# Kernel tuning notes

Hardware: AMD Instinct MI355X
Metric: run time of the kernel (lower is better)

The kernel has to match this reference:

```python
import jax, jax.numpy as jnp
import numpy as np

VOCAB = 100000
EMB = 300
HID = 512            # bidirectional total; per-direction = 256
HD = HID // 2
TAGS = 12
START = 10
STOP = 11
NEG = -10000.0
T = 4096


def _lstm_dir(x, h0, c0, Wih, Whh, bih, bhh, reverse):
    # x: [T, EMB]; PyTorch gate order i, f, g, o
    def step(carry, xt):
        h, c = carry
        g = xt @ Wih.T + h @ Whh.T + bih + bhh           # [4*HD]
        i, f, gg, o = jnp.split(g, 4)
        i = jax.nn.sigmoid(i); f = jax.nn.sigmoid(f)
        gg = jnp.tanh(gg); o = jax.nn.sigmoid(o)
        c = f * c + i * gg
        h = o * jnp.tanh(c)
        return (h, c), h
    _, hs = jax.lax.scan(step, (h0, c0), x, reverse=reverse)
    return hs                                            # [T, HD]


def setup_inputs() -> dict:
    key = jax.random.key(0)
    ks = jax.random.split(key, 16)
    s = 0.05  # weight scale for numerical stability
    sentence = jax.random.randint(ks[0], (T,), 0, VOCAB)
    h0 = jax.random.normal(ks[1], (2, HD), jnp.float32)
    c0 = jax.random.normal(ks[2], (2, HD), jnp.float32)
    embed = jax.random.normal(ks[3], (VOCAB, EMB), jnp.float32) * s
    W_ih_f = jax.random.normal(ks[4], (4 * HD, EMB), jnp.float32) * s
    W_hh_f = jax.random.normal(ks[5], (4 * HD, HD), jnp.float32) * s
    b_ih_f = jax.random.normal(ks[6], (4 * HD,), jnp.float32) * s
    b_hh_f = jax.random.normal(ks[7], (4 * HD,), jnp.float32) * s
    W_ih_b = jax.random.normal(ks[8], (4 * HD, EMB), jnp.float32) * s
    W_hh_b = jax.random.normal(ks[9], (4 * HD, HD), jnp.float32) * s
    b_ih_b = jax.random.normal(ks[10], (4 * HD,), jnp.float32) * s
    b_hh_b = jax.random.normal(ks[11], (4 * HD,), jnp.float32) * s
    W_tag = jax.random.normal(ks[12], (TAGS, HID), jnp.float32) * s
    b_tag = jax.random.normal(ks[13], (TAGS,), jnp.float32) * s
    transitions = jax.random.normal(ks[14], (TAGS, TAGS), jnp.float32)
    transitions = transitions.at[START, :].set(NEG).at[:, STOP].set(NEG)
    return dict(sentence=sentence, h0=h0, c0=c0, embed=embed,
                W_ih_f=W_ih_f, W_hh_f=W_hh_f, b_ih_f=b_ih_f, b_hh_f=b_hh_f,
                W_ih_b=W_ih_b, W_hh_b=W_hh_b, b_ih_b=b_ih_b, b_hh_b=b_hh_b,
                W_tag=W_tag, b_tag=b_tag, transitions=transitions)


def reference(sentence, h0, c0, embed,
              W_ih_f, W_hh_f, b_ih_f, b_hh_f,
              W_ih_b, W_hh_b, b_ih_b, b_hh_b,
              W_tag, b_tag, transitions):
    # --- BiLSTM features (dropout layers are identity at inference) ---
    x = embed[sentence]                                      # [T, EMB]
    hf = _lstm_dir(x, h0[0], c0[0], W_ih_f, W_hh_f, b_ih_f, b_hh_f, False)
    hb = _lstm_dir(x, h0[1], c0[1], W_ih_b, W_hh_b, b_ih_b, b_hh_b, True)
    feats = jnp.concatenate([hf, hb], axis=-1) @ W_tag.T + b_tag  # [T, TAGS]

    # --- Viterbi decode: transitions[to, from] ---
    init = jnp.full((TAGS,), NEG, jnp.float32).at[START].set(0.0)

    def vstep(fv, feat):
        ntv = fv[None, :] + transitions                      # [to, from]
        bp = jnp.argmax(ntv, axis=1)                         # best prev tag per 'to'
        fv2 = jnp.max(ntv, axis=1) + feat
        return fv2, bp

    fv, bps = jax.lax.scan(vstep, init, feats)               # bps: [T, TAGS]
    terminal = fv + transitions[STOP]
    best = jnp.argmax(terminal)
    path_score = terminal[best]

    def back(tag, bp):
        return bp[tag], tag

    _, best_path = jax.lax.scan(back, best, bps, reverse=True)  # [T] tags in time order
    return path_score, best_path
```

## Files before the change

### kernel.cpp

```cpp
#include <hip/hip_runtime.h>

#define T_LEN 4096
#define EMB   300
#define HD    256
#define G4    1024
#define N2    2048
#define TAGS  12
#define NEGV  -10000.0f
#define SENT  0x7F7F7F7Fu

__global__ __launch_bounds__(256) void gin_gemm(
    const int* __restrict__ sent, const float* __restrict__ embed,
    const float* __restrict__ Wf, const float* __restrict__ Wb,
    const float* __restrict__ bihf, const float* __restrict__ bhhf,
    const float* __restrict__ bihb, const float* __restrict__ bhhb,
    float* __restrict__ gin)
{
    __shared__ float AsT[32][68];
    __shared__ float BsT[32][68];
    __shared__ int   sIdx[64];
    const int tid = threadIdx.x;
    const int bn = blockIdx.x;
    const int bm = blockIdx.y;
    if (tid < 64) sIdx[tid] = sent[bm*64 + tid];
    __syncthreads();

    float acc[4][4] = {};
    const int lr = tid >> 3;
    const int lk = (tid & 7) << 2;
    const int m0 = (tid >> 4) << 2;
    const int n0 = (tid & 15) << 2;

    for (int kc = 0; kc < 10; ++kc) {
        const int k0 = kc*32 + lk;
        #pragma unroll
        for (int h = 0; h < 2; ++h) {
            const int row = lr + h*32;
            float4 va = make_float4(0.f,0.f,0.f,0.f);
            if (k0 + 3 < EMB)
                va = *(const float4*)(embed + (long)sIdx[row]*EMB + k0);
            AsT[lk+0][row]=va.x; AsT[lk+1][row]=va.y;
            AsT[lk+2][row]=va.z; AsT[lk+3][row]=va.w;

            const int rn = bn*64 + row;
            const float* bsrc = (rn < G4) ? (Wf + (long)rn*EMB) : (Wb + (long)(rn-G4)*EMB);
            float4 vb = make_float4(0.f,0.f,0.f,0.f);
            if (k0 + 3 < EMB)
                vb = *(const float4*)(bsrc + k0);
            BsT[lk+0][row]=vb.x; BsT[lk+1][row]=vb.y;
            BsT[lk+2][row]=vb.z; BsT[lk+3][row]=vb.w;
        }
        __syncthreads();
        #pragma unroll
        for (int kk = 0; kk < 32; ++kk) {
            const float4 a4 = *(const float4*)&AsT[kk][m0];
            const float4 b4 = *(const float4*)&BsT[kk][n0];
            const float a[4] = {a4.x, a4.y, a4.z, a4.w};
            const float b[4] = {b4.x, b4.y, b4.z, b4.w};
            #pragma unroll
            for (int i = 0; i < 4; ++i)
                #pragma unroll
                for (int jj = 0; jj < 4; ++jj)
                    acc[i][jj] = fmaf(a[i], b[jj], acc[i][jj]);
        }
        __syncthreads();
    }

    #pragma unroll
    for (int i = 0; i < 4; ++i) {
        const int t = bm*64 + m0 + i;
        #pragma unroll
        for (int jj = 0; jj < 4; ++jj) {
            const int r = bn*64 + n0 + jj;
            const float bias = (r < G4) ? (bihf[r] + bhhf[r])
                                        : (bihb[r-G4] + bhhb[r-G4]);
            gin[(long)t*N2 + r] = acc[i][jj] + bias;
        }
    }
}

#define MV(K) { const float4 hv = h4[K];                    \
    a0 = fmaf(wA##K.x, hv.x, a0);                           \
    a1 = fmaf(wA##K.y, hv.y, a1);                           \
    a2 = fmaf(wA##K.z, hv.z, a2);                           \
    a3 = fmaf(wA##K.w, hv.w, a3); }

__global__ __launch_bounds__(1024) __attribute__((amdgpu_waves_per_eu(4, 4)))
void lstm_persist(
    const float* Whh_f, const float* Whh_b,
    const float* __restrict__ h0, const float* __restrict__ c0,
    const float* __restrict__ gin,
    float* Hh)
{
    const int blk = blockIdx.x;
    const int m8  = blk & 7;
    if (m8 != 0 && m8 != 4) return;
    const int dir = (m8 == 4);
    const int b   = blk >> 3;
    const int tid = threadIdx.x;
    const int u     = tid & 63;
    const int wvid  = tid >> 6;
    const int gate  = wvid >> 2;
    const int q     = wvid & 3;
    const int unit0 = b*64;
    const int row   = gate*64 + u;
    const int grow  = gate*HD + unit0 + u;

    const float4* W4 = (const float4*)((dir ? Whh_b : Whh_f)
                                       + (long)grow*HD + q*64);
    const float4 wA0  = W4[0],  wA1  = W4[1],  wA2  = W4[2],  wA3  = W4[3];
    const float4 wA4  = W4[4],  wA5  = W4[5],  wA6  = W4[6],  wA7  = W4[7];
    const float4 wA8  = W4[8],  wA9  = W4[9],  wA10 = W4[10], wA11 = W4[11];
    const float4 wA12 = W4[12], wA13 = W4[13], wA14 = W4[14], wA15 = W4[15];

    __shared__ __align__(16) float hS[20480];
    __shared__ float ps[3][256];
    __shared__ float gvS[256];

    float cst = 0.f;
    if (tid < 64) cst = c0[dir*HD + unit0 + tid];
    if (tid < HD) hS[tid] = h0[dir*HD + tid];

    const float* ginD = gin + dir*G4;
    float gx = (q == 0) ? ginD[(long)(dir ? T_LEN-1 : 0)*N2 + grow] : 0.f;

    #pragma unroll 1
    for (int s = 0; s < T_LEN; ++s) {
        const int t = dir ? (T_LEN-1-s) : s;
        float gxn = 0.f;
        if (q == 0 && s+1 < T_LEN)
            gxn = ginD[(long)(dir ? t-1 : t+1)*N2 + grow];

        __syncthreads();
        const float4* h4 = (const float4*)(hS + q*64);
        float a0=0.f, a1=0.f, a2=0.f, a3=0.f;
        MV(0)  MV(1)  MV(2)  MV(3)
        MV(4)  MV(5)  MV(6)  MV(7)
        MV(8)  MV(9)  MV(10) MV(11)
        MV(12) MV(13) MV(14) MV(15)
        const float a = (a0+a1)+(a2+a3);

        if (q != 0) ps[q-1][row] = a;
        __syncthreads();

        if (q == 0) {
            const float raw = a + ps[0][row] + ps[1][row] + ps[2][row] + gx;
            gvS[row] = (gate == 2) ? tanhf(raw) : 1.f/(1.f + expf(-raw));
        }
        __syncthreads();

        if (tid < 64) {
            const float i_ = gvS[tid],       f_ = gvS[64+tid];
            const float g_ = gvS[128+tid],   o_ = gvS[192+tid];
            cst = fmaf(f_, cst, i_*g_);
            const float hv = o_ * tanhf(cst);
            hS[unit0 + tid] = hv;
            __hip_atomic_store(&Hh[(long)t*512 + dir*HD + unit0 + tid], hv,
                               __ATOMIC_RELAXED, __HIP_MEMORY_SCOPE_AGENT);
        } else if (tid < 256 && s+1 < T_LEN) {
            const int fidx = tid - 64;
            const int gu   = (fidx < unit0) ? fidx : fidx + 64;
            const long idx = (long)t*512 + dir*HD + gu;
            float v;
            do {
                v = __hip_atomic_load(&Hh[idx], __ATOMIC_RELAXED,
                                      __HIP_MEMORY_SCOPE_AGENT);
            } while (__float_as_uint(v) == SENT);
            hS[gu] = v;
        }
        gx = gxn;
    }
}

__global__ __launch_bounds__(192) void feats_kernel(
    const float* __restrict__ Hhist, const float* __restrict__ Wtag,
    const float* __restrict__ btag, float* __restrict__ feats)
{
    __shared__ __align__(16) float Ws[TAGS][512];
    const int tid = threadIdx.x;
    for (int i = tid; i < TAGS*512; i += 192) Ws[0][i] = Wtag[i];
    __syncthreads();
    const int tl = tid / TAGS;
    const int tg = tid % TAGS;
    const int t  = blockIdx.x * 16 + tl;
    const float4* hrow = (const float4*)(Hhist + (long)t*512);
    const float4* wrow = (const float4*)(&Ws[tg][0]);
    float a0=0.f,a1=0.f,a2=0.f,a3=0.f;
    #pragma unroll 8
    for (int k = 0; k < 128; ++k) {
        const float4 h = hrow[k];
        const float4 ww = wrow[k];
        a0=fmaf(h.x,ww.x,a0); a1=fmaf(h.y,ww.y,a1);
        a2=fmaf(h.z,ww.z,a2); a3=fmaf(h.w,ww.w,a3);
    }
    feats[t*TAGS + tg] = ((a0+a1)+(a2+a3)) + btag[tg];
}

__global__ __launch_bounds__(256) void viterbi_kernel(
    const float* __restrict__ feats, const float* __restrict__ trans,
    float* __restrict__ out)
{
    __shared__ float fS[256*TAGS];
    __shared__ unsigned char bps[T_LEN*TAGS];
    __shared__ float fvS[TAGS];
    const int tid = threadIdx.x;

    float tr[TAGS];
    float fv = NEGV;
    if (tid < TAGS) {
        #pragma unroll
        for (int f = 0; f < TAGS; ++f) tr[f] = trans[tid*TAGS + f];
        fv = (tid == 10) ? 0.f : NEGV;
    }

    for (int c = 0; c < T_LEN/256; ++c) {
        __syncthreads();
        for (int i = tid; i < 256*TAGS; i += 256) fS[i] = feats[c*256*TAGS + i];
        __syncthreads();
        if (tid < TAGS) {
            for (int s = 0; s < 256; ++s) {
                float best = -3.4e38f; int bp = 0;
                #pragma unroll
                for (int f = 0; f < TAGS; ++f) {
                    const float v = __shfl(fv, f, 64) + tr[f];
                    if (v > best) { best = v; bp = f; }
                }
                bps[(c*256+s)*TAGS + tid] = (unsigned char)bp;
                fv = best + fS[s*TAGS + tid];
            }
        }
    }
    __syncthreads();
    if (tid < TAGS) fvS[tid] = fv + trans[11*TAGS + tid];
    __syncthreads();
    if (tid == 0) {
        float bestv = fvS[0]; int best = 0;
        #pragma unroll
        for (int g = 1; g < TAGS; ++g) if (fvS[g] > bestv) { bestv = fvS[g]; best = g; }
        out[0] = bestv;
        int cur = best;
        for (int t = T_LEN-1; t >= 0; --t) {
            out[1+t] = (float)cur;
            cur = bps[t*TAGS + cur];
        }
    }
}

extern "C" void kernel_launch(void* const* d_in, const int* in_sizes, int n_in,
                              void* d_out, int out_size, void* d_ws, size_t ws_size,
                              hipStream_t stream)
{
    (void)in_sizes; (void)n_in; (void)out_size; (void)ws_size;
    const int*   sentence = (const int*)  d_in[0];
    const float* h0       = (const float*)d_in[1];
    const float* c0       = (const float*)d_in[2];
    const float* embed    = (const float*)d_in[3];
    const float* Wihf     = (const float*)d_in[4];
    const float* Whhf     = (const float*)d_in[5];
    const float* bihf     = (const float*)d_in[6];
    const float* bhhf     = (const float*)d_in[7];
    const float* Wihb     = (const float*)d_in[8];
    const float* Whhb     = (const float*)d_in[9];
    const float* bihb     = (const float*)d_in[10];
    const float* bhhb     = (const float*)d_in[11];
    const float* Wtag     = (const float*)d_in[12];
    const float* btag     = (const float*)d_in[13];
    const float* trans    = (const float*)d_in[14];
    float* out = (float*)d_out;

    float* gin   = (float*)d_ws;
    float* Hh    = gin + (long)T_LEN*N2;
    float* feats = Hh  + (long)T_LEN*512;

    hipMemsetAsync(Hh, 0x7F, (size_t)T_LEN*512*sizeof(float), stream);

    dim3 ggrid(32, 64);
    gin_gemm<<<ggrid, 256, 0, stream>>>(sentence, embed, Wihf, Wihb,
                                        bihf, bhhf, bihb, bhhb, gin);
    lstm_persist<<<29, 1024, 0, stream>>>(Whhf, Whhb, h0, c0, gin, Hh);
    feats_kernel<<<T_LEN/16, 192, 0, stream>>>(Hh, Wtag, btag, feats);
    viterbi_kernel<<<1, 256, 0, stream>>>(feats, trans, out);
}
```

Before: 7.204 ms.

## Split LSTM recurrence by K-slices across blocks and exchange partial sums

The recurrent matvec is repartitioned so each of four blocks per direction owns a 64-wide slice of the hidden input for all 1024 gate rows, instead of owning 64 output units. Blocks exchange partial dot products through a ring of global slots guarded by sentinels. Each block then redundantly computes the full gate nonlinearity and cell update locally, which drops the per-step all-gather of hidden state and one intra-block barrier. In exchange every block polls three remote partial buffers each step. Slot reuse correctness rests on a sentinel written eight steps ahead.

```diff
diff --git a/kernel.cpp b/kernel.cpp
--- a/kernel.cpp
+++ b/kernel.cpp
@@ -8,6 +8,7 @@
 #define TAGS  12
 #define NEGV  -10000.0f
 #define SENT  0x7F7F7F7Fu
+#define NSLOT 16
 
 __global__ __launch_bounds__(256) void gin_gemm(
     const int* __restrict__ sent, const float* __restrict__ embed,
@@ -85,12 +86,13 @@
     a2 = fmaf(wA##K.z, hv.z, a2);                           \
     a3 = fmaf(wA##K.w, hv.w, a3); }
 
-__global__ __launch_bounds__(1024) __attribute__((amdgpu_waves_per_eu(4, 4)))
+__global__ __launch_bounds__(1024, 4)
 void lstm_persist(
-    const float* Whh_f, const float* Whh_b,
+    const float* __restrict__ Whh_f, const float* __restrict__ Whh_b,
     const float* __restrict__ h0, const float* __restrict__ c0,
     const float* __restrict__ gin,
-    float* Hh)
+    float* __restrict__ Hh,
+    float* __restrict__ Pbuf)
 {
     const int blk = blockIdx.x;
     const int m8  = blk & 7;
@@ -98,41 +100,40 @@
     const int dir = (m8 == 4);
     const int b   = blk >> 3;
     const int tid = threadIdx.x;
-    const int u     = tid & 63;
-    const int wvid  = tid >> 6;
-    const int gate  = wvid >> 2;
-    const int q     = wvid & 3;
-    const int unit0 = b*64;
-    const int row   = gate*64 + u;
-    const int grow  = gate*HD + unit0 + u;
+    const int gate = tid >> 8;
 
     const float4* W4 = (const float4*)((dir ? Whh_b : Whh_f)
-                                       + (long)grow*HD + q*64);
+                                       + (long)tid*HD + b*64);
     const float4 wA0  = W4[0],  wA1  = W4[1],  wA2  = W4[2],  wA3  = W4[3];
     const float4 wA4  = W4[4],  wA5  = W4[5],  wA6  = W4[6],  wA7  = W4[7];
     const float4 wA8  = W4[8],  wA9  = W4[9],  wA10 = W4[10], wA11 = W4[11];
     const float4 wA12 = W4[12], wA13 = W4[13], wA14 = W4[14], wA15 = W4[15];
 
     __shared__ __align__(16) float hS[20480];
-    __shared__ float ps[3][256];
-    __shared__ float gvS[256];
+    __shared__ float gvS[G4];
 
     float cst = 0.f;
-    if (tid < 64) cst = c0[dir*HD + unit0 + tid];
-    if (tid < HD) hS[tid] = h0[dir*HD + tid];
+    if (tid < HD) {
+        cst = c0[dir*HD + tid];
+        hS[tid] = h0[dir*HD + tid];
+    }
+    __syncthreads();
 
     const float* ginD = gin + dir*G4;
-    float gx = (q == 0) ? ginD[(long)(dir ? T_LEN-1 : 0)*N2 + grow] : 0.f;
+    float gx = ginD[(long)(dir ? T_LEN-1 : 0)*N2 + tid];
+
+    const int f0 = (b == 0) ? 1 : 0;
+    const int f1 = (b <= 1) ? 2 : 1;
+    const int f2 = (b <= 2) ? 3 : 2;
 
     #pragma unroll 1
     for (int s = 0; s < T_LEN; ++s) {
         const int t = dir ? (T_LEN-1-s) : s;
         float gxn = 0.f;
-        if (q == 0 && s+1 < T_LEN)
-            gxn = ginD[(long)(dir ? t-1 : t+1)*N2 + grow];
-
-        __syncthreads();
-        const float4* h4 = (const float4*)(hS + q*64);
+        if (s+1 < T_LEN)
+            gxn = ginD[(long)(dir ? t-1 : t+1)*N2 + tid];
+
+        const float4* h4 = (const float4*)(hS + b*64);
         float a0=0.f, a1=0.f, a2=0.f, a3=0.f;
         MV(0)  MV(1)  MV(2)  MV(3)
         MV(4)  MV(5)  MV(6)  MV(7)
@@ -140,34 +141,48 @@
         MV(12) MV(13) MV(14) MV(15)
         const float a = (a0+a1)+(a2+a3);
 
-        if (q != 0) ps[q-1][row] = a;
-        __syncthreads();
-
-        if (q == 0) {
-            const float raw = a + ps[0][row] + ps[1][row] + ps[2][row] + gx;
-            gvS[row] = (gate == 2) ? tanhf(raw) : 1.f/(1.f + expf(-raw));
-        }
-        __syncthreads();
-
-        if (tid < 64) {
-            const float i_ = gvS[tid],       f_ = gvS[64+tid];
-            const float g_ = gvS[128+tid],   o_ = gvS[192+tid];
+        const long sb  = ((long)((s & (NSLOT-1))*2 + dir))*4096;
+        const long sbf = ((long)((((s+8) & (NSLOT-1))*2) + dir))*4096;
+        __hip_atomic_store(&Pbuf[sb  + b*1024 + tid], a,
+                           __ATOMIC_RELAXED, __HIP_MEMORY_SCOPE_AGENT);
+        __hip_atomic_store(&Pbuf[sbf + b*1024 + tid], __uint_as_float(SENT),
+                           __ATOMIC_RELAXED, __HIP_MEMORY_SCOPE_AGENT);
+
+        float* P0 = Pbuf + sb + f0*1024 + tid;
+        float* P1 = Pbuf + sb + f1*1024 + tid;
+        float* P2 = Pbuf + sb + f2*1024 + tid;
+        float v0 = 0.f, v1 = 0.f, v2 = 0.f;
+        bool d0 = false, d1 = false, d2 = false;
+        do {
+            if (!d0) { v0 = __hip_atomic_load(P0, __ATOMIC_RELAXED,
+                                              __HIP_MEMORY_SCOPE_AGENT);
+                       d0 = (__float_as_uint(v0) != SENT); }
+            if (!d1) { v1 = __hip_atomic_load(P1, __ATOMIC_RELAXED,
+                                              __HIP_MEMORY_SCOPE_AGENT);
+                       d1 = (__float_as_uint(v1) != SENT); }
+            if (!d2) { v2 = __hip_atomic_load(P2, __ATOMIC_RELAXED,
+                                              __HIP_MEMORY_SCOPE_AGENT);
+                       d2 = (__float_as_uint(v2) != SENT); }
+        } while (!(d0 && d1 && d2));
+
+        const float pos0 = (b == 0) ? a : v0;
+        const float pos1 = (b == 1) ? a : ((b == 0) ? v0 : v1);
+        const float pos2 = (b == 2) ? a : ((b <= 1) ? v1 : v2);
+        const float pos3 = (b == 3) ? a : v2;
+        const float g = ((pos0 + pos1) + (pos2 + pos3)) + gx;
+        gvS[tid] = (gate == 2) ? tanhf(g) : 1.f/(1.f + expf(-g));
+        __syncthreads();
+
+        if (tid < HD) {
+            const float i_ = gvS[tid],        f_ = gvS[HD + tid];
+            const float g_ = gvS[2*HD + tid], o_ = gvS[3*HD + tid];
             cst = fmaf(f_, cst, i_*g_);
             const float hv = o_ * tanhf(cst);
-            hS[unit0 + tid] = hv;
-            __hip_atomic_store(&Hh[(long)t*512 + dir*HD + unit0 + tid], hv,
-                               __ATOMIC_RELAXED, __HIP_MEMORY_SCOPE_AGENT);
-        } else if (tid < 256 && s+1 < T_LEN) {
-            const int fidx = tid - 64;
-            const int gu   = (fidx < unit0) ? fidx : fidx + 64;
-            const long idx = (long)t*512 + dir*HD + gu;
-            float v;
-            do {
-                v = __hip_atomic_load(&Hh[idx], __ATOMIC_RELAXED,
-                                      __HIP_MEMORY_SCOPE_AGENT);
-            } while (__float_as_uint(v) == SENT);
-            hS[gu] = v;
-        }
+            hS[tid] = hv;
+            if (b == 0)
+                Hh[(long)t*512 + dir*HD + tid] = hv;
+        }
+        __syncthreads();
         gx = gxn;
     }
 }
@@ -269,15 +284,16 @@
     float* out = (float*)d_out;
 
     float* gin   = (float*)d_ws;
-    float* Hh    = gin + (long)T_LEN*N2;
-    float* feats = Hh  + (long)T_LEN*512;
-
-    hipMemsetAsync(Hh, 0x7F, (size_t)T_LEN*512*sizeof(float), stream);
+    float* Hh    = gin   + (long)T_LEN*N2;
+    float* feats = Hh    + (long)T_LEN*512;
+    float* Pbuf  = feats + (long)T_LEN*TAGS;
+
+    hipMemsetAsync(Pbuf, 0x7F, (size_t)NSLOT*2*4*1024*sizeof(float), stream);
 
     dim3 ggrid(32, 64);
     gin_gemm<<<ggrid, 256, 0, stream>>>(sentence, embed, Wihf, Wihb,
                                         bihf, bhhf, bihb, bhhb, gin);
-    lstm_persist<<<29, 1024, 0, stream>>>(Whhf, Whhb, h0, c0, gin, Hh);
+    lstm_persist<<<29, 1024, 0, stream>>>(Whhf, Whhb, h0, c0, gin, Hh, Pbuf);
     feats_kernel<<<T_LEN/16, 192, 0, stream>>>(Hh, Wtag, btag, feats);
     viterbi_kernel<<<1, 256, 0, stream>>>(feats, trans, out);
 }
```

New measurement: 9.777 ms. 1.36x slower.

## Fuse input-projection GEMM into persistent LSTM kernel with sentinel-polled readiness

Applied to the files above, without the earlier changes.

Merges the input-gate GEMM and the persistent recurrent LSTM into one launch. Extra blocks compute GEMM tiles in an order alternating from both ends of the sequence, so the forward and backward directions get their early timesteps first. The recurrent blocks poll gin for a sentinel value before using it, which lets the GEMM overlap the serial recurrence and removes the separate GEMM launch. The trade-offs are a full gin memset, atomic loads and spin loops in the recurrence, and 145KB of shared memory for every block. GEMM blocks now use 1024 threads each computing a 2x2 tile, and there is a forward-progress risk if the LSTM blocks are not scheduled before the GEMM blocks.

```diff
diff --git a/kernel.cpp b/kernel.cpp
--- a/kernel.cpp
+++ b/kernel.cpp
@@ -8,76 +8,7 @@
 #define TAGS  12
 #define NEGV  -10000.0f
 #define SENT  0x7F7F7F7Fu
-
-__global__ __launch_bounds__(256) void gin_gemm(
-    const int* __restrict__ sent, const float* __restrict__ embed,
-    const float* __restrict__ Wf, const float* __restrict__ Wb,
-    const float* __restrict__ bihf, const float* __restrict__ bhhf,
-    const float* __restrict__ bihb, const float* __restrict__ bhhb,
-    float* __restrict__ gin)
-{
-    __shared__ float AsT[32][68];
-    __shared__ float BsT[32][68];
-    __shared__ int   sIdx[64];
-    const int tid = threadIdx.x;
-    const int bn = blockIdx.x;
-    const int bm = blockIdx.y;
-    if (tid < 64) sIdx[tid] = sent[bm*64 + tid];
-    __syncthreads();
-
-    float acc[4][4] = {};
-    const int lr = tid >> 3;
-    const int lk = (tid & 7) << 2;
-    const int m0 = (tid >> 4) << 2;
-    const int n0 = (tid & 15) << 2;
-
-    for (int kc = 0; kc < 10; ++kc) {
-        const int k0 = kc*32 + lk;
-        #pragma unroll
-        for (int h = 0; h < 2; ++h) {
-            const int row = lr + h*32;
-            float4 va = make_float4(0.f,0.f,0.f,0.f);
-            if (k0 + 3 < EMB)
-                va = *(const float4*)(embed + (long)sIdx[row]*EMB + k0);
-            AsT[lk+0][row]=va.x; AsT[lk+1][row]=va.y;
-            AsT[lk+2][row]=va.z; AsT[lk+3][row]=va.w;
-
-            const int rn = bn*64 + row;
-            const float* bsrc = (rn < G4) ? (Wf + (long)rn*EMB) : (Wb + (long)(rn-G4)*EMB);
-            float4 vb = make_float4(0.f,0.f,0.f,0.f);
-            if (k0 + 3 < EMB)
-                vb = *(const float4*)(bsrc + k0);
-            BsT[lk+0][row]=vb.x; BsT[lk+1][row]=vb.y;
-            BsT[lk+2][row]=vb.z; BsT[lk+3][row]=vb.w;
-        }
-        __syncthreads();
-        #pragma unroll
-        for (int kk = 0; kk < 32; ++kk) {
-            const float4 a4 = *(const float4*)&AsT[kk][m0];
-            const float4 b4 = *(const float4*)&BsT[kk][n0];
-            const float a[4] = {a4.x, a4.y, a4.z, a4.w};
-            const float b[4] = {b4.x, b4.y, b4.z, b4.w};
-            #pragma unroll
-            for (int i = 0; i < 4; ++i)
-                #pragma unroll
-                for (int jj = 0; jj < 4; ++jj)
-                    acc[i][jj] = fmaf(a[i], b[jj], acc[i][jj]);
-        }
-        __syncthreads();
-    }
-
-    #pragma unroll
-    for (int i = 0; i < 4; ++i) {
-        const int t = bm*64 + m0 + i;
-        #pragma unroll
-        for (int jj = 0; jj < 4; ++jj) {
-            const int r = bn*64 + n0 + jj;
-            const float bias = (r < G4) ? (bihf[r] + bhhf[r])
-                                        : (bihb[r-G4] + bhhb[r-G4]);
-            gin[(long)t*N2 + r] = acc[i][jj] + bias;
-        }
-    }
-}
+#define NLSTM 29
 
 #define MV(K) { const float4 hv = h4[K];                    \
     a0 = fmaf(wA##K.x, hv.x, a0);                           \
@@ -85,19 +16,87 @@
     a2 = fmaf(wA##K.z, hv.z, a2);                           \
     a3 = fmaf(wA##K.w, hv.w, a3); }
 
-__global__ __launch_bounds__(1024) __attribute__((amdgpu_waves_per_eu(4, 4)))
-void lstm_persist(
+__global__ __launch_bounds__(1024) void fused_gemm_lstm(
+    const int* __restrict__ sent, const float* __restrict__ embed,
+    const float* __restrict__ Wihf, const float* __restrict__ Wihb,
+    const float* __restrict__ bihf, const float* __restrict__ bhhf,
+    const float* __restrict__ bihb, const float* __restrict__ bhhb,
     const float* Whh_f, const float* Whh_b,
     const float* __restrict__ h0, const float* __restrict__ c0,
-    const float* __restrict__ gin,
+    float* gin,
     float* Hh)
 {
+    __shared__ __align__(16) char smem[145*1024];
     const int blk = blockIdx.x;
-    const int m8  = blk & 7;
+    const int tid = threadIdx.x;
+
+    if (blk >= NLSTM) {
+        float* AsT  = (float*)smem;
+        float* BsT  = (float*)(smem + 8704);
+        int*   sIdx = (int*)  (smem + 17408);
+        const int g  = blk - NLSTM;
+        const int kk8 = g >> 5;
+        const int bn  = g & 31;
+        const int bm  = (kk8 & 1) ? (63 - (kk8 >> 1)) : (kk8 >> 1);
+
+        if (tid < 64) sIdx[tid] = sent[bm*64 + tid];
+        __syncthreads();
+
+        const int srow = tid >> 4;
+        const int skj  = (tid & 15) << 1;
+        const int m0   = (tid >> 5) << 1;
+        const int n0   = (tid & 31) << 1;
+        const int rn   = bn * 64;
+        float acc00=0.f, acc01=0.f, acc10=0.f, acc11=0.f;
+
+        for (int kc = 0; kc < 10; ++kc) {
+            const int k0 = kc*32 + skj;
+            float2 va = make_float2(0.f, 0.f), vb = make_float2(0.f, 0.f);
+            if (k0 + 1 < EMB) {
+                va = *(const float2*)(embed + (long)sIdx[srow]*EMB + k0);
+                const int r = rn + srow;
+                const float* bsrc = (r < G4) ? (Wihf + (long)r*EMB)
+                                             : (Wihb + (long)(r-G4)*EMB);
+                vb = *(const float2*)(bsrc + k0);
+            }
+            AsT[skj*68 + srow]     = va.x;
+            AsT[(skj+1)*68 + srow] = va.y;
+            BsT[skj*68 + srow]     = vb.x;
+            BsT[(skj+1)*68 + srow] = vb.y;
+            __syncthreads();
+            #pragma unroll
+            for (int kk = 0; kk < 32; ++kk) {
+                const float2 a2v = *(const float2*)&AsT[kk*68 + m0];
+                const float2 b2v = *(const float2*)&BsT[kk*68 + n0];
+                acc00 = fmaf(a2v.x, b2v.x, acc00);
+                acc01 = fmaf(a2v.x, b2v.y, acc01);
+                acc10 = fmaf(a2v.y, b2v.x, acc10);
+                acc11 = fmaf(a2v.y, b2v.y, acc11);
+            }
+            __syncthreads();
+        }
+
+        const int c0i = rn + n0, c1i = c0i + 1;
+        const float bias0 = (c0i < G4) ? (bihf[c0i] + bhhf[c0i])
+                                       : (bihb[c0i-G4] + bhhb[c0i-G4]);
+        const float bias1 = (c1i < G4) ? (bihf[c1i] + bhhf[c1i])
+                                       : (bihb[c1i-G4] + bhhb[c1i-G4]);
+        const long t0 = (long)(bm*64 + m0), t1 = t0 + 1;
+        __hip_atomic_store(&gin[t0*N2 + c0i], acc00 + bias0,
+                           __ATOMIC_RELAXED, __HIP_MEMORY_SCOPE_AGENT);
+        __hip_atomic_store(&gin[t0*N2 + c1i], acc01 + bias1,
+                           __ATOMIC_RELAXED, __HIP_MEMORY_SCOPE_AGENT);
+        __hip_atomic_store(&gin[t1*N2 + c0i], acc10 + bias0,
+                           __ATOMIC_RELAXED, __HIP_MEMORY_SCOPE_AGENT);
+        __hip_atomic_store(&gin[t1*N2 + c1i], acc11 + bias1,
+                           __ATOMIC_RELAXED, __HIP_MEMORY_SCOPE_AGENT);
+        return;
+    }
+
+    const int m8 = blk & 7;
     if (m8 != 0 && m8 != 4) return;
     const int dir = (m8 == 4);
     const int b   = blk >> 3;
-    const int tid = threadIdx.x;
     const int u     = tid & 63;
     const int wvid  = tid >> 6;
     const int gate  = wvid >> 2;
@@ -106,6 +105,10 @@
     const int row   = gate*64 + u;
     const int grow  = gate*HD + unit0 + u;
 
+    float* hS  = (float*)smem;
+    float* ps  = (float*)(smem + 1024);
+    float* gvS = (float*)(smem + 4096);
+
     const float4* W4 = (const float4*)((dir ? Whh_b : Whh_f)
                                        + (long)grow*HD + q*64);
     const float4 wA0  = W4[0],  wA1  = W4[1],  wA2  = W4[2],  wA3  = W4[3];
@@ -113,23 +116,31 @@
     const float4 wA8  = W4[8],  wA9  = W4[9],  wA10 = W4[10], wA11 = W4[11];
     const float4 wA12 = W4[12], wA13 = W4[13], wA14 = W4[14], wA15 = W4[15];
 
-    __shared__ __align__(16) float hS[20480];
-    __shared__ float ps[3][256];
-    __shared__ float gvS[256];
-
     float cst = 0.f;
     if (tid < 64) cst = c0[dir*HD + unit0 + tid];
     if (tid < HD) hS[tid] = h0[dir*HD + tid];
 
-    const float* ginD = gin + dir*G4;
-    float gx = (q == 0) ? ginD[(long)(dir ? T_LEN-1 : 0)*N2 + grow] : 0.f;
+    float* ginD = gin + dir*G4;
+    float gx;
+    {
+        const long gi0 = (long)(dir ? T_LEN-1 : 0)*N2 + grow;
+        do {
+            gx = __hip_atomic_load(&ginD[gi0], __ATOMIC_RELAXED,
+                                   __HIP_MEMORY_SCOPE_AGENT);
+        } while (__float_as_uint(gx) == SENT);
+    }
 
     #pragma unroll 1
     for (int s = 0; s < T_LEN; ++s) {
         const int t = dir ? (T_LEN-1-s) : s;
         float gxn = 0.f;
-        if (q == 0 && s+1 < T_LEN)
-            gxn = ginD[(long)(dir ? t-1 : t+1)*N2 + grow];
+        long  gidx = 0;
+        if (s+1 < T_LEN) {
+            gidx = (long)(dir ? t-1 : t+1)*N2 + grow;
+            gxn = __hip_atomic_load(&ginD[gidx], __ATOMIC_RELAXED,
+                                    __HIP_MEMORY_SCOPE_AGENT);
+            __builtin_amdgcn_sched_barrier(0);
+        }
 
         __syncthreads();
         const float4* h4 = (const float4*)(hS + q*64);
@@ -139,12 +150,11 @@
         MV(8)  MV(9)  MV(10) MV(11)
         MV(12) MV(13) MV(14) MV(15)
         const float a = (a0+a1)+(a2+a3);
-
-        if (q != 0) ps[q-1][row] = a;
+        if (q != 0) ps[(q-1)*256 + row] = a;
         __syncthreads();
 
         if (q == 0) {
-            const float raw = a + ps[0][row] + ps[1][row] + ps[2][row] + gx;
+            const float raw = a + ps[row] + ps[256+row] + ps[512+row] + gx;
             gvS[row] = (gate == 2) ? tanhf(raw) : 1.f/(1.f + expf(-raw));
         }
         __syncthreads();
@@ -168,6 +178,12 @@
             } while (__float_as_uint(v) == SENT);
             hS[gu] = v;
         }
+
+        if (s+1 < T_LEN) {
+            while (__float_as_uint(gxn) == SENT)
+                gxn = __hip_atomic_load(&ginD[gidx], __ATOMIC_RELAXED,
+                                        __HIP_MEMORY_SCOPE_AGENT);
+        }
         gx = gxn;
     }
 }
@@ -272,12 +288,12 @@
     float* Hh    = gin + (long)T_LEN*N2;
     float* feats = Hh  + (long)T_LEN*512;
 
-    hipMemsetAsync(Hh, 0x7F, (size_t)T_LEN*512*sizeof(float), stream);
-
-    dim3 ggrid(32, 64);
-    gin_gemm<<<ggrid, 256, 0, stream>>>(sentence, embed, Wihf, Wihb,
-                                        bihf, bhhf, bihb, bhhb, gin);
-    lstm_persist<<<29, 1024, 0, stream>>>(Whhf, Whhb, h0, c0, gin, Hh);
+    hipMemsetAsync(gin, 0x7F, (size_t)T_LEN*N2*sizeof(float), stream);
+    hipMemsetAsync(Hh,  0x7F, (size_t)T_LEN*512*sizeof(float), stream);
+
+    fused_gemm_lstm<<<NLSTM + 2048, 1024, 0, stream>>>(
+        sentence, embed, Wihf, Wihb, bihf, bhhf, bihb, bhhb,
+        Whhf, Whhb, h0, c0, gin, Hh);
     feats_kernel<<<T_LEN/16, 192, 0, stream>>>(Hh, Wtag, btag, feats);
     viterbi_kernel<<<1, 256, 0, stream>>>(feats, trans, out);
 }
```

New measurement: 7.332 ms. No clear change (+1.8%).
